# Kernel tuning notes

Measured on AMD Instinct MI355X. Metric: run time of the kernel, lower is better.

Reference implementation:

```python
import jax, jax.numpy as jnp
import numpy as np

H = 16        # query heads
KV = 4        # key/value heads
HD = 64       # head dim
BASE = 10000.0
SCALE = HD ** (-0.5) * 0.8


def setup_inputs() -> dict:
    key = jax.random.key(0)
    ks = jax.random.split(key, 5)
    B, S, D = 2, 4096, 1024
    return {
        "hidden_states": jax.random.normal(ks[0], (B, S, D), dtype=jnp.float32),
        "wq": jax.random.normal(ks[1], (D, H * HD), dtype=jnp.float32) * (D ** -0.5),
        "wk": jax.random.normal(ks[2], (D, KV * HD), dtype=jnp.float32) * (D ** -0.5),
        "wv": jax.random.normal(ks[3], (D, KV * HD), dtype=jnp.float32) * (D ** -0.5),
        "wo": jax.random.normal(ks[4], (H * HD, D), dtype=jnp.float32) * ((H * HD) ** -0.5),
    }


def _rope_tables(seq_len, dtype):
    inv_freq = 1.0 / (BASE ** (jnp.arange(0, HD, 2, dtype=jnp.float32) / HD))
    t = jnp.arange(seq_len, dtype=jnp.float32)
    freqs = t[:, None] * inv_freq[None, :]            # [S, HD/2]
    emb = jnp.concatenate([freqs, freqs], axis=-1)    # [S, HD]
    return jnp.cos(emb).astype(dtype), jnp.sin(emb).astype(dtype)


def _rotate_half(x):
    x1, x2 = x[..., : HD // 2], x[..., HD // 2 :]
    return jnp.concatenate([-x2, x1], axis=-1)


def reference(hidden_states, wq, wk, wv, wo):
    B, S, D = hidden_states.shape
    G = H // KV
    q = (hidden_states @ wq).reshape(B, S, H, HD).transpose(0, 2, 1, 3)   # [B,H,S,HD]
    k = (hidden_states @ wk).reshape(B, S, KV, HD).transpose(0, 2, 1, 3)  # [B,KV,S,HD]
    v = (hidden_states @ wv).reshape(B, S, KV, HD).transpose(0, 2, 1, 3)
    cos, sin = _rope_tables(S, q.dtype)               # [S,HD] each
    cos = cos[None, None]                             # [1,1,S,HD]
    sin = sin[None, None]
    q = q * cos + _rotate_half(q) * sin
    k = k * cos + _rotate_half(k) * sin
    k = jnp.repeat(k, G, axis=1)                      # [B,H,S,HD]
    v = jnp.repeat(v, G, axis=1)
    scores = jnp.einsum("bhqd,bhkd->bhqk", q, k) * SCALE
    probs = jax.nn.softmax(scores.astype(jnp.float32), axis=-1).astype(q.dtype)
    out = jnp.einsum("bhqk,bhkd->bhqd", probs, v)     # [B,H,S,HD]
    out = out.transpose(0, 2, 1, 3).reshape(B, S, H * HD)
    return out @ wo
```

## Files before the change

kernel.cpp:

```cpp
#include <hip/hip_runtime.h>
#include <hip/hip_fp16.h>
#include <math.h>

typedef _Float16 f16;
typedef _Float16 half8 __attribute__((ext_vector_type(8)));
typedef _Float16 half4v __attribute__((ext_vector_type(4)));
typedef _Float16 half2v __attribute__((ext_vector_type(2)));
typedef float f32x4 __attribute__((ext_vector_type(4)));
typedef float f32x16 __attribute__((ext_vector_type(16)));
typedef unsigned uint2v __attribute__((ext_vector_type(2)));

#define NB 2
#define NS 4096
#define ND 1024
#define NH 16
#define NKV 4
#define NHD 64
#define ATT_SCALE2 0.14426950408889634f

__global__ __launch_bounds__(256) void wprep_k(
    const float* __restrict__ wq, const float* __restrict__ wk,
    const float* __restrict__ wv, const float* __restrict__ wo,
    f16* __restrict__ Bt, f16* __restrict__ Wot)
{
  __shared__ f16 tile[64][72];
  int bx = blockIdx.x, by = blockIdx.y;
  const float* src; int ldn, colbase, nbase; f16* dst;
  if (bx < 24) {
    int n0 = bx * 64;
    if (n0 < 1024)      { src = wq; ldn = 1024; colbase = n0; }
    else if (n0 < 1280) { src = wk; ldn = 256;  colbase = n0 - 1024; }
    else                { src = wv; ldn = 256;  colbase = n0 - 1280; }
    dst = Bt; nbase = n0;
  } else {
    src = wo; ldn = 1024; colbase = (bx - 24) * 64; dst = Wot; nbase = (bx - 24) * 64;
  }
  int tid = threadIdx.x;
  int kr = tid >> 4;
  int nc = (tid & 15) * 4;
  #pragma unroll
  for (int i = 0; i < 4; ++i) {
    int k = by * 64 + kr + i * 16;
    float4 v = *reinterpret_cast<const float4*>(src + (size_t)k * ldn + colbase + nc);
    tile[nc + 0][kr + i * 16] = (f16)v.x;
    tile[nc + 1][kr + i * 16] = (f16)v.y;
    tile[nc + 2][kr + i * 16] = (f16)v.z;
    tile[nc + 3][kr + i * 16] = (f16)v.w;
  }
  __syncthreads();
  int nl = tid >> 2;
  int kb = (tid & 3) * 16;
  half8 a = *reinterpret_cast<const half8*>(&tile[nl][kb]);
  half8 b = *reinterpret_cast<const half8*>(&tile[nl][kb + 8]);
  f16* o = dst + (size_t)(nbase + nl) * 1024 + by * 64 + kb;
  *reinterpret_cast<half8*>(o) = a;
  *reinterpret_cast<half8*>(o + 8) = b;
}

template<int MODE>
__global__ __launch_bounds__(256) void gemm_k(
    const float* __restrict__ Af32, const f16* __restrict__ Af16,
    const f16* __restrict__ Bt,
    f16* __restrict__ q_h, f16* __restrict__ k_h, f16* __restrict__ vT_h,
    float* __restrict__ outp)
{
  __shared__ f16 As[128 * 32];
  __shared__ f16 Bs[128 * 32];
  int tid = threadIdx.x;
  int lane = tid & 63, w = tid >> 6;
  int wr = w >> 1, wc = w & 1;
  int g = lane >> 4, lr = lane & 15;
  int m0 = blockIdx.y * 128, n0 = blockIdx.x * 128;

  f32x4 acc[4][4] = {};

  int ar = tid >> 1;
  int ac = (tid & 1) * 16;

  for (int k0 = 0; k0 < ND; k0 += 32) {
    if (MODE == 0) {
      const float* Ap = Af32 + (size_t)(m0 + ar) * ND + k0 + ac;
      #pragma unroll
      for (int i = 0; i < 4; ++i) {
        float4 v = *reinterpret_cast<const float4*>(Ap + i * 4);
        int col = ac + i * 4;
        int slot = (col >> 3) ^ (ar & 3);
        half4v hv = { (f16)v.x, (f16)v.y, (f16)v.z, (f16)v.w };
        *reinterpret_cast<half4v*>(&As[ar * 32 + slot * 8 + (col & 7)]) = hv;
      }
    } else {
      const f16* Ap = Af16 + (size_t)(m0 + ar) * ND + k0 + ac;
      half8 v0 = *reinterpret_cast<const half8*>(Ap);
      half8 v1 = *reinterpret_cast<const half8*>(Ap + 8);
      int s0 = (ac >> 3) ^ (ar & 3);
      int s1 = ((ac >> 3) + 1) ^ (ar & 3);
      *reinterpret_cast<half8*>(&As[ar * 32 + s0 * 8]) = v0;
      *reinterpret_cast<half8*>(&As[ar * 32 + s1 * 8]) = v1;
    }
    {
      const f16* Bp = Bt + (size_t)(n0 + ar) * ND + k0 + ac;
      half8 v0 = *reinterpret_cast<const half8*>(Bp);
      half8 v1 = *reinterpret_cast<const half8*>(Bp + 8);
      int s0 = (ac >> 3) ^ (ar & 3);
      int s1 = ((ac >> 3) + 1) ^ (ar & 3);
      *reinterpret_cast<half8*>(&Bs[ar * 32 + s0 * 8]) = v0;
      *reinterpret_cast<half8*>(&Bs[ar * 32 + s1 * 8]) = v1;
    }
    __syncthreads();
    half8 af[4], bf[4];
    #pragma unroll
    for (int mt = 0; mt < 4; ++mt) {
      int row = wr * 64 + mt * 16 + lr;
      af[mt] = *reinterpret_cast<const half8*>(&As[row * 32 + (g ^ (row & 3)) * 8]);
    }
    #pragma unroll
    for (int nt = 0; nt < 4; ++nt) {
      int row = wc * 64 + nt * 16 + lr;
      bf[nt] = *reinterpret_cast<const half8*>(&Bs[row * 32 + (g ^ (row & 3)) * 8]);
    }
    #pragma unroll
    for (int mt = 0; mt < 4; ++mt)
      #pragma unroll
      for (int nt = 0; nt < 4; ++nt)
        acc[mt][nt] = __builtin_amdgcn_mfma_f32_16x16x32_f16(af[mt], bf[nt], acc[mt][nt], 0, 0, 0);
    __syncthreads();
  }

  #pragma unroll
  for (int mt = 0; mt < 4; ++mt)
    #pragma unroll
    for (int nt = 0; nt < 4; ++nt)
      #pragma unroll
      for (int r = 0; r < 4; ++r) {
        int m = m0 + wr * 64 + mt * 16 + g * 4 + r;
        int n = n0 + wc * 64 + nt * 16 + lr;
        float val = acc[mt][nt][r];
        if (MODE == 0) {
          int b = m >> 12, s = m & (NS - 1);
          f16 hv = (f16)val;
          if (n < 1024)      q_h[(((size_t)b * NH + (n >> 6)) * NS + s) * NHD + (n & 63)] = hv;
          else if (n < 1280) { int nn = n - 1024; k_h[(((size_t)b * NKV + (nn >> 6)) * NS + s) * NHD + (nn & 63)] = hv; }
          else               { int nn = n - 1280; vT_h[(((size_t)b * NKV + (nn >> 6)) * NHD + (nn & 63)) * NS + s] = hv; }
        } else {
          outp[(size_t)m * ND + n] = val;
        }
      }
}

__global__ __launch_bounds__(256) void rope_k(f16* __restrict__ q_h, f16* __restrict__ k_h)
{
  __shared__ float cs[16][33], sn[16][33];
  int b = blockIdx.y;
  int s0 = blockIdx.x * 16;
  int tid = threadIdx.x;
  for (int idx = tid; idx < 512; idx += 256) {
    int sl = idx >> 5, d = idx & 31;
    double inv = exp((double)d * -0.28782313662425575);
    double ang = (double)(s0 + sl) * inv;
    cs[sl][d] = (float)cos(ang);
    sn[sl][d] = (float)sin(ang);
  }
  __syncthreads();
  for (int p = tid; p < 512 * 20; p += 256) {
    int u = p >> 9; int rem = p & 511; int sl = rem >> 5; int d = rem & 31;
    f16* ptr;
    if (u < NH) ptr = q_h + (((size_t)b * NH + u) * NS + s0 + sl) * NHD;
    else        ptr = k_h + (((size_t)b * NKV + (u - NH)) * NS + s0 + sl) * NHD;
    float x1 = (float)ptr[d], x2 = (float)ptr[d + 32];
    float c = cs[sl][d], si = sn[sl][d];
    ptr[d]      = (f16)(x1 * c - x2 * si);
    ptr[d + 32] = (f16)(x2 * c + x1 * si);
  }
}

__global__ __launch_bounds__(512) void attn_k(
    const f16* __restrict__ q_h, const f16* __restrict__ k_h,
    const f16* __restrict__ vT_h, f16* __restrict__ attn_h)
{
  __shared__ f16 Ks[2][64 * 64];
  __shared__ f16 Vs[2][64 * 64];
  int tid = threadIdx.x;
  int lane = tid & 63, w = tid >> 6;
  int hi = lane >> 5, qr = lane & 31;
  int bh = blockIdx.x; int b = bh >> 4, h = bh & 15, kvh = h >> 2;
  int q0 = blockIdx.y * 256 + w * 32;

  const f16* qptr = q_h + (((size_t)b * NH + h) * NS + q0 + qr) * NHD + hi * 8;
  half8 qf[4];
  #pragma unroll
  for (int ks = 0; ks < 4; ++ks)
    qf[ks] = *reinterpret_cast<const half8*>(qptr + 16 * ks);

  const f16* kbase = k_h + ((size_t)b * NKV + kvh) * NS * NHD;
  const f16* vbase = vT_h + ((size_t)b * NKV + kvh) * NHD * NS;

  f32x16 accO[2] = {};
  float m_run = 0.0f;
  float l_lane = 0.f;

  int srow = tid >> 3;
  int scol = (tid & 7) * 8;
  int sslot = ((scol >> 3) ^ (srow & 7)) * 8;
  int qs = qr & 7;

  {
    half8 kv0 = *reinterpret_cast<const half8*>(kbase + (size_t)srow * NHD + scol);
    half8 vv0 = *reinterpret_cast<const half8*>(vbase + (size_t)srow * NS + scol);
    *reinterpret_cast<half8*>(&Ks[0][srow * 64 + sslot]) = kv0;
    *reinterpret_cast<half8*>(&Vs[0][srow * 64 + sslot]) = vv0;
  }

  const half2v ones2 = { (f16)1.0f, (f16)1.0f };

  unsigned wrd[2][4][2];

#define SMCHUNK(KB, SC, E, LACC) do { \
    float a0_ = exp2f(fmaf((SC)[(E) * 4 + 0], ATT_SCALE2, -m_run)); \
    float a1_ = exp2f(fmaf((SC)[(E) * 4 + 1], ATT_SCALE2, -m_run)); \
    unsigned u0_ = __builtin_bit_cast(unsigned, __builtin_amdgcn_cvt_pkrtz(a0_, a1_)); \
    wrd[KB][E][0] = u0_; \
    LACC = __builtin_amdgcn_fdot2(__builtin_bit_cast(half2v, u0_), ones2, LACC, false); \
    float a2_ = exp2f(fmaf((SC)[(E) * 4 + 2], ATT_SCALE2, -m_run)); \
    float a3_ = exp2f(fmaf((SC)[(E) * 4 + 3], ATT_SCALE2, -m_run)); \
    unsigned u1_ = __builtin_bit_cast(unsigned, __builtin_amdgcn_cvt_pkrtz(a2_, a3_)); \
    wrd[KB][E][1] = u1_; \
    LACC = __builtin_amdgcn_fdot2(__builtin_bit_cast(half2v, u1_), ones2, LACC, false); \
  } while (0)

#define QK1STEP(KS) do { \
    int cs_ = 2 * (KS) + hi; \
    half8 kf1_ = *reinterpret_cast<const half8*>(&Kc[(32 + qr) * 64 + ((cs_ ^ qs) << 3)]); \
    __builtin_amdgcn_s_setprio(1); \
    sc1 = __builtin_amdgcn_mfma_f32_32x32x16_f16(kf1_, qf[KS], sc1, 0, 0, 0); \
    __builtin_amdgcn_s_setprio(0); \
  } while (0)

#define PVSTEP(KS) do { \
    int kb_ = (KS) >> 1, e0_ = 2 * ((KS) & 1); \
    uint2v s0_ = __builtin_amdgcn_permlane32_swap(wrd[kb_][e0_][0], wrd[kb_][e0_ + 1][0], false, false); \
    uint2v s1_ = __builtin_amdgcn_permlane32_swap(wrd[kb_][e0_][1], wrd[kb_][e0_ + 1][1], false, false); \
    union { unsigned u[4]; half8 h; } pfu_; \
    pfu_.u[0] = s0_[0]; pfu_.u[1] = s1_[0]; pfu_.u[2] = s0_[1]; pfu_.u[3] = s1_[1]; \
    int cs_ = 2 * (KS) + hi; \
    half8 vf0_ = *reinterpret_cast<const half8*>(&Vc[qr * 64 + ((cs_ ^ qs) << 3)]); \
    half8 vf1_ = *reinterpret_cast<const half8*>(&Vc[(32 + qr) * 64 + ((cs_ ^ qs) << 3)]); \
    __builtin_amdgcn_s_setprio(1); \
    accO[0] = __builtin_amdgcn_mfma_f32_32x32x16_f16(vf0_, pfu_.h, accO[0], 0, 0, 0); \
    accO[1] = __builtin_amdgcn_mfma_f32_32x32x16_f16(vf1_, pfu_.h, accO[1], 0, 0, 0); \
    __builtin_amdgcn_s_setprio(0); \
  } while (0)

  int cur = 0;
  for (int t = 0; t < 64; ++t) {
    __syncthreads();
    int tn = (t < 63) ? t + 1 : t;
    int kt2 = tn * 64;
    half8 kreg = *reinterpret_cast<const half8*>(kbase + (size_t)(kt2 + srow) * NHD + scol);
    half8 vreg = *reinterpret_cast<const half8*>(vbase + (size_t)srow * NS + kt2 + scol);

    const f16* Kc = &Ks[cur][0];
    const f16* Vc = &Vs[cur][0];

    f32x16 sc0 = {}, sc1 = {};
    #pragma unroll
    for (int ks = 0; ks < 4; ++ks) {
      int cs = 2 * ks + hi;
      half8 kf0 = *reinterpret_cast<const half8*>(&Kc[qr * 64 + ((cs ^ qs) << 3)]);
      __builtin_amdgcn_s_setprio(1);
      sc0 = __builtin_amdgcn_mfma_f32_32x32x16_f16(kf0, qf[ks], sc0, 0, 0, 0);
      __builtin_amdgcn_s_setprio(0);
    }

    float l0 = 0.f, l1 = 0.f;
    QK1STEP(0); SMCHUNK(0, sc0, 0, l0);
    QK1STEP(1); SMCHUNK(0, sc0, 1, l0);
    QK1STEP(2); SMCHUNK(0, sc0, 2, l0);
    QK1STEP(3); SMCHUNK(0, sc0, 3, l0);

    PVSTEP(0);  SMCHUNK(1, sc1, 0, l1);
    PVSTEP(1);  SMCHUNK(1, sc1, 1, l1);
    PVSTEP(2);  SMCHUNK(1, sc1, 2, l1);
    SMCHUNK(1, sc1, 3, l1);
    PVSTEP(3);

    float ltile = l0 + l1;
    l_lane += ltile;

    if (__any(ltile > 16384.0f)) {
      const float alpha = 0x1p-16f;
      #pragma unroll
      for (int db = 0; db < 2; ++db)
        #pragma unroll
        for (int i = 0; i < 16; ++i) accO[db][i] *= alpha;
      l_lane *= alpha;
      m_run += 16.0f;
    }

    *reinterpret_cast<half8*>(&Ks[cur ^ 1][srow * 64 + sslot]) = kreg;
    *reinterpret_cast<half8*>(&Vs[cur ^ 1][srow * 64 + sslot]) = vreg;
    cur ^= 1;
  }
#undef SMCHUNK
#undef QK1STEP
#undef PVSTEP

  float l_tot = l_lane + __shfl_xor(l_lane, 32);
  float inv_l = 1.0f / l_tot;
  f16* obase = attn_h + ((size_t)b * NS + q0 + qr) * ND + h * NHD;
  #pragma unroll
  for (int db = 0; db < 2; ++db)
    #pragma unroll
    for (int e = 0; e < 4; ++e) {
      half4v ov = { (f16)(accO[db][e * 4 + 0] * inv_l), (f16)(accO[db][e * 4 + 1] * inv_l),
                    (f16)(accO[db][e * 4 + 2] * inv_l), (f16)(accO[db][e * 4 + 3] * inv_l) };
      *reinterpret_cast<half4v*>(obase + db * 32 + e * 8 + hi * 4) = ov;
    }
}

extern "C" void kernel_launch(void* const* d_in, const int* in_sizes, int n_in,
                              void* d_out, int out_size, void* d_ws, size_t ws_size,
                              hipStream_t stream)
{
  (void)in_sizes; (void)n_in; (void)out_size; (void)ws_size;
  const float* hs = (const float*)d_in[0];
  const float* wq = (const float*)d_in[1];
  const float* wk = (const float*)d_in[2];
  const float* wv = (const float*)d_in[3];
  const float* wo = (const float*)d_in[4];
  float* outp = (float*)d_out;

  f16* q_h    = (f16*)d_ws;
  f16* k_h    = q_h    + (size_t)NB * NH * NS * NHD;
  f16* vT_h   = k_h    + (size_t)NB * NKV * NS * NHD;
  f16* attn_h = vT_h   + (size_t)NB * NKV * NS * NHD;
  f16* Bt     = attn_h + (size_t)NB * NS * ND;
  f16* Wot    = Bt     + (size_t)1536 * 1024;

  wprep_k<<<dim3(40, 16), 256, 0, stream>>>(wq, wk, wv, wo, Bt, Wot);
  gemm_k<0><<<dim3(12, 64), 256, 0, stream>>>(hs, nullptr, Bt, q_h, k_h, vT_h, nullptr);
  rope_k<<<dim3(256, 2), 256, 0, stream>>>(q_h, k_h);
  attn_k<<<dim3(32, 16), 512, 0, stream>>>(q_h, k_h, vT_h, attn_h);
  gemm_k<1><<<dim3(8, 64), 256, 0, stream>>>(nullptr, attn_h, Wot, nullptr, nullptr, nullptr, outp);
}
```

Measured before the change: 325.3 us.

## Fuse RoPE into QKV projection epilogue using precomputed cos/sin table

Removes the separate RoPE kernel, which re-read and rewrote all of Q and K in fp16. The GEMM epilogue now pairs accumulator columns d and d+32, which sit in the same thread's tiles, and applies the rotation before storing. A cos/sin table is computed by extra blocks in the weight-prep kernel and stored in the attention-output workspace. That buffer is only overwritten later by attention, so the reuse is safe. The epilogue reads the table from global memory per element, adding some load traffic in exchange for one fewer launch and full Q/K pass.

```diff
diff --git a/kernel.cpp b/kernel.cpp
--- a/kernel.cpp
+++ b/kernel.cpp
@@ -21,10 +21,24 @@
 __global__ __launch_bounds__(256) void wprep_k(
     const float* __restrict__ wq, const float* __restrict__ wk,
     const float* __restrict__ wv, const float* __restrict__ wo,
-    f16* __restrict__ Bt, f16* __restrict__ Wot)
+    f16* __restrict__ Bt, f16* __restrict__ Wot, float* __restrict__ ropet)
 {
   __shared__ f16 tile[64][72];
   int bx = blockIdx.x, by = blockIdx.y;
+  int tid = threadIdx.x;
+  if (bx >= 40) {
+    int e0 = (((bx - 40) * 16 + by) * 256 + tid) * 4;
+    #pragma unroll
+    for (int i = 0; i < 4; ++i) {
+      int e = e0 + i;
+      int s = e >> 5, d = e & 31;
+      double inv = exp((double)d * -0.28782313662425575);
+      double ang = (double)s * inv;
+      ropet[e]          = (float)cos(ang);
+      ropet[131072 + e] = (float)sin(ang);
+    }
+    return;
+  }
   const float* src; int ldn, colbase, nbase; f16* dst;
   if (bx < 24) {
     int n0 = bx * 64;
@@ -35,7 +49,6 @@
   } else {
     src = wo; ldn = 1024; colbase = (bx - 24) * 64; dst = Wot; nbase = (bx - 24) * 64;
   }
-  int tid = threadIdx.x;
   int kr = tid >> 4;
   int nc = (tid & 15) * 4;
   #pragma unroll
@@ -60,7 +73,7 @@
 template<int MODE>
 __global__ __launch_bounds__(256) void gemm_k(
     const float* __restrict__ Af32, const f16* __restrict__ Af16,
-    const f16* __restrict__ Bt,
+    const f16* __restrict__ Bt, const float* __restrict__ ropet,
     f16* __restrict__ q_h, f16* __restrict__ k_h, f16* __restrict__ vT_h,
     float* __restrict__ outp)
 {
@@ -126,50 +139,51 @@
     __syncthreads();
   }
 
-  #pragma unroll
-  for (int mt = 0; mt < 4; ++mt)
-    #pragma unroll
-    for (int nt = 0; nt < 4; ++nt)
+  if (MODE == 0) {
+    #pragma unroll
+    for (int mt = 0; mt < 4; ++mt)
       #pragma unroll
       for (int r = 0; r < 4; ++r) {
         int m = m0 + wr * 64 + mt * 16 + g * 4 + r;
-        int n = n0 + wc * 64 + nt * 16 + lr;
-        float val = acc[mt][nt][r];
-        if (MODE == 0) {
-          int b = m >> 12, s = m & (NS - 1);
-          f16 hv = (f16)val;
-          if (n < 1024)      q_h[(((size_t)b * NH + (n >> 6)) * NS + s) * NHD + (n & 63)] = hv;
-          else if (n < 1280) { int nn = n - 1024; k_h[(((size_t)b * NKV + (nn >> 6)) * NS + s) * NHD + (nn & 63)] = hv; }
-          else               { int nn = n - 1280; vT_h[(((size_t)b * NKV + (nn >> 6)) * NHD + (nn & 63)) * NS + s] = hv; }
-        } else {
-          outp[(size_t)m * ND + n] = val;
+        int b = m >> 12, s = m & (NS - 1);
+        #pragma unroll
+        for (int nt = 0; nt < 2; ++nt) {
+          int n_lo = n0 + wc * 64 + nt * 16 + lr;
+          float x1 = acc[mt][nt][r];
+          float x2 = acc[mt][nt + 2][r];
+          if (n_lo < 1280) {
+            int d = nt * 16 + lr;
+            float c  = ropet[s * 32 + d];
+            float si = ropet[131072 + s * 32 + d];
+            f16 o1 = (f16)(x1 * c - x2 * si);
+            f16 o2 = (f16)(x2 * c + x1 * si);
+            if (n_lo < 1024) {
+              f16* qp = q_h + (((size_t)b * NH + (n_lo >> 6)) * NS + s) * NHD + d;
+              qp[0] = o1; qp[32] = o2;
+            } else {
+              int nn = n_lo - 1024;
+              f16* kp = k_h + (((size_t)b * NKV + (nn >> 6)) * NS + s) * NHD + d;
+              kp[0] = o1; kp[32] = o2;
+            }
+          } else {
+            int nn = n_lo - 1280;
+            f16* vp = vT_h + (((size_t)b * NKV + (nn >> 6)) * NHD + (nn & 63)) * NS + s;
+            vp[0] = (f16)x1;
+            vp[32 * NS] = (f16)x2;
+          }
         }
       }
-}
-
-__global__ __launch_bounds__(256) void rope_k(f16* __restrict__ q_h, f16* __restrict__ k_h)
-{
-  __shared__ float cs[16][33], sn[16][33];
-  int b = blockIdx.y;
-  int s0 = blockIdx.x * 16;
-  int tid = threadIdx.x;
-  for (int idx = tid; idx < 512; idx += 256) {
-    int sl = idx >> 5, d = idx & 31;
-    double inv = exp((double)d * -0.28782313662425575);
-    double ang = (double)(s0 + sl) * inv;
-    cs[sl][d] = (float)cos(ang);
-    sn[sl][d] = (float)sin(ang);
-  }
-  __syncthreads();
-  for (int p = tid; p < 512 * 20; p += 256) {
-    int u = p >> 9; int rem = p & 511; int sl = rem >> 5; int d = rem & 31;
-    f16* ptr;
-    if (u < NH) ptr = q_h + (((size_t)b * NH + u) * NS + s0 + sl) * NHD;
-    else        ptr = k_h + (((size_t)b * NKV + (u - NH)) * NS + s0 + sl) * NHD;
-    float x1 = (float)ptr[d], x2 = (float)ptr[d + 32];
-    float c = cs[sl][d], si = sn[sl][d];
-    ptr[d]      = (f16)(x1 * c - x2 * si);
-    ptr[d + 32] = (f16)(x2 * c + x1 * si);
+  } else {
+    #pragma unroll
+    for (int mt = 0; mt < 4; ++mt)
+      #pragma unroll
+      for (int nt = 0; nt < 4; ++nt)
+        #pragma unroll
+        for (int r = 0; r < 4; ++r) {
+          int m = m0 + wr * 64 + mt * 16 + g * 4 + r;
+          int n = n0 + wc * 64 + nt * 16 + lr;
+          outp[(size_t)m * ND + n] = acc[mt][nt][r];
+        }
   }
 }
 
@@ -335,10 +349,10 @@
   f16* attn_h = vT_h   + (size_t)NB * NKV * NS * NHD;
   f16* Bt     = attn_h + (size_t)NB * NS * ND;
   f16* Wot    = Bt     + (size_t)1536 * 1024;
-
-  wprep_k<<<dim3(40, 16), 256, 0, stream>>>(wq, wk, wv, wo, Bt, Wot);
-  gemm_k<0><<<dim3(12, 64), 256, 0, stream>>>(hs, nullptr, Bt, q_h, k_h, vT_h, nullptr);
-  rope_k<<<dim3(256, 2), 256, 0, stream>>>(q_h, k_h);
+  float* ropet = (float*)attn_h;
+
+  wprep_k<<<dim3(48, 16), 256, 0, stream>>>(wq, wk, wv, wo, Bt, Wot, ropet);
+  gemm_k<0><<<dim3(12, 64), 256, 0, stream>>>(hs, nullptr, Bt, ropet, q_h, k_h, vT_h, nullptr);
   attn_k<<<dim3(32, 16), 512, 0, stream>>>(q_h, k_h, vT_h, attn_h);
-  gemm_k<1><<<dim3(8, 64), 256, 0, stream>>>(nullptr, attn_h, Wot, nullptr, nullptr, nullptr, outp);
+  gemm_k<1><<<dim3(8, 64), 256, 0, stream>>>(nullptr, attn_h, Wot, nullptr, nullptr, nullptr, nullptr, outp);
 }
```

Result: faster. 315.4 us (median of 2 runs) (-3.0%).
